# Kernel tuning notes

Hardware: AMD Instinct MI355X
Metric: run time of the kernel (lower is better)

Reference implementation:

```python
import jax, jax.numpy as jnp
import numpy as np

NUM_GROUPS = 16
MINIS_PER_GROUP = 16
MINIS_PER_TOK = 4
HIDDEN = 8192
N_TOKENS = 8192


def setup_inputs() -> dict:
    key = jax.random.key(0)
    k1, k2, k3 = jax.random.split(key, 3)
    hidden_states = jax.random.normal(k1, (N_TOKENS, HIDDEN), dtype=jnp.float32)
    # nn.Linear weight: [num_groups, hidden]
    group_gate_w = jax.random.normal(k2, (NUM_GROUPS, HIDDEN), dtype=jnp.float32) * 0.02
    # mini_gates parameter: [num_groups, hidden, minis_per_group]
    mini_gates = jax.random.normal(k3, (NUM_GROUPS, HIDDEN, MINIS_PER_GROUP), dtype=jnp.float32) * 0.02
    return {"hidden_states": hidden_states, "group_gate_w": group_gate_w, "mini_gates": mini_gates}


def reference(hidden_states, group_gate_w, mini_gates):
    # Tier 1: group gate
    group_logits = hidden_states @ group_gate_w.T                      # [N, G]
    group_probs = jax.nn.softmax(group_logits.astype(jnp.float32), axis=-1)
    top_group_probs = jnp.max(group_probs, axis=-1)                    # [N]
    top_group_indices = jnp.argmax(group_probs, axis=-1)               # [N]

    # Tier 2: per-token mini-gate. Instead of gathering a huge [N, H, E]
    # tensor (as the torch code does), compute logits for ALL groups
    # ([N, G, E] is tiny) and select the chosen group's row — same math.
    all_mini_logits = jnp.einsum('nh,ghe->nge', hidden_states, mini_gates)  # [N, G, E]
    mini_logits = jnp.take_along_axis(
        all_mini_logits, top_group_indices[:, None, None], axis=1
    )[:, 0, :]                                                         # [N, E]
    mini_probs = jax.nn.softmax(mini_logits.astype(jnp.float32), axis=-1)

    topk_mini_probs, topk_mini_indices = jax.lax.top_k(mini_probs, MINIS_PER_TOK)
    final_probs = top_group_probs[:, None] * topk_mini_probs
    final_probs = final_probs / jnp.sum(final_probs, axis=-1, keepdims=True)

    global_expert_indices = top_group_indices[:, None] * MINIS_PER_GROUP + topk_mini_indices

    group_aux_loss = jnp.sum(jnp.mean(group_probs, axis=0) ** 2)
    mini_aux_loss = jnp.sum(jnp.mean(mini_probs, axis=0) ** 2)
    total_aux_loss = group_aux_loss + mini_aux_loss

    return (final_probs.astype(hidden_states.dtype), global_expert_indices, total_aux_loss)
```

## Files before the change

### kernel.cpp

```cpp
#include <hip/hip_runtime.h>
#include <math.h>

#define N_TOK 8192
#define HID   8192
#define NG    16
#define NE    16
#define KC    512
#define NCHUNK (HID / KC)
#define TPB   8

#define OFF_CNT   0u
#define OFF_GSUM  64u
#define OFF_ESUM  128u
#define OFF_NTIL  192u
#define ZERO_BYTES 256u
#define OFF_GLOG  256u
#define OFF_MLOG  (OFF_GLOG + N_TOK*NG*8)
#define OFF_TOPG  (OFF_MLOG + N_TOK*NE*8)
#define OFF_BUCK  (OFF_TOPG + N_TOK*4)
#define OFF_SCHED (OFF_BUCK + NG*N_TOK*4)
#define OFF_MGT   (OFF_SCHED + 2048*4)

__device__ __forceinline__ void glds16(const float* gp, float* lp) {
    __builtin_amdgcn_global_load_lds(
        (const __attribute__((address_space(1))) void*)gp,
        (__attribute__((address_space(3))) void*)lp, 16, 0, 0);
}

#define RS_ROUND(o, half)                                                 \
  {                                                                       \
    const bool hi_ = (lane & (o)) != 0;                                   \
    _Pragma("unroll")                                                     \
    for (int i_ = 0; i_ < (half); ++i_) {                                 \
      double s_ = hi_ ? acc64[i_] : acc64[i_ + (half)];                   \
      double r_ = __shfl_xor(s_, (o));                                    \
      acc64[i_] = (hi_ ? acc64[i_ + (half)] : acc64[i_]) + r_;            \
    }                                                                     \
  }

__global__ __launch_bounds__(256, 2) void k_group(
    const float* __restrict__ hid, const float* __restrict__ gw,
    double* __restrict__ glog)
{
    __shared__ float Wl[2][NG * KC];
    const int tid  = threadIdx.x;
    const int lane = tid & 63;
    const int wv   = tid >> 6;
    const int t0   = blockIdx.x * TPB + wv * 2;
    const float* __restrict__ a0 = hid + (size_t)t0 * HID;
    const float* __restrict__ a1 = a0 + HID;

    #pragma unroll
    for (int j = 0; j < 8; ++j) {
        int m = wv * 8 + j;
        glds16(gw + (size_t)(m >> 1) * HID + (m & 1) * 256 + 4 * lane,
               &Wl[0][m * 256]);
    }
    float4 areg[4];
    areg[0] = *(const float4*)&a0[4 * lane];
    areg[1] = *(const float4*)&a0[256 + 4 * lane];
    areg[2] = *(const float4*)&a1[4 * lane];
    areg[3] = *(const float4*)&a1[256 + 4 * lane];

    double acc64[32];
    #pragma unroll
    for (int i = 0; i < 32; ++i) acc64[i] = 0.0;

    for (int c = 0; c < NCHUNK; ++c) {
        __syncthreads();
        float4 aC0 = areg[0], aC1 = areg[1], aC2 = areg[2], aC3 = areg[3];
        if (c + 1 < NCHUNK) {
            const int kb = (c + 1) * KC;
            #pragma unroll
            for (int j = 0; j < 8; ++j) {
                int m = wv * 8 + j;
                glds16(gw + (size_t)(m >> 1) * HID + kb + (m & 1) * 256 + 4 * lane,
                       &Wl[(c + 1) & 1][m * 256]);
            }
            areg[0] = *(const float4*)&a0[kb + 4 * lane];
            areg[1] = *(const float4*)&a0[kb + 256 + 4 * lane];
            areg[2] = *(const float4*)&a1[kb + 4 * lane];
            areg[3] = *(const float4*)&a1[kb + 256 + 4 * lane];
        }
        const float* Wc = &Wl[c & 1][0];
        #pragma unroll
        for (int g = 0; g < NG; ++g) {
            float4 w0 = *(const float4*)&Wc[g * KC + 4 * lane];
            float4 w1 = *(const float4*)&Wc[g * KC + 256 + 4 * lane];
            float d0 = aC0.x*w0.x + aC0.y*w0.y + aC0.z*w0.z + aC0.w*w0.w
                     + aC1.x*w1.x + aC1.y*w1.y + aC1.z*w1.z + aC1.w*w1.w;
            float d1 = aC2.x*w0.x + aC2.y*w0.y + aC2.z*w0.z + aC2.w*w0.w
                     + aC3.x*w1.x + aC3.y*w1.y + aC3.z*w1.z + aC3.w*w1.w;
            acc64[g]      += (double)d0;
            acc64[16 + g] += (double)d1;
        }
    }

    #pragma unroll
    for (int i = 0; i < 32; ++i) acc64[i] += __shfl_xor(acc64[i], 32);
    RS_ROUND(16, 16) RS_ROUND(8, 8) RS_ROUND(4, 4) RS_ROUND(2, 2) RS_ROUND(1, 1)
    if (lane < 32)
        glog[(size_t)(t0 + (lane >> 4)) * NG + (lane & 15)] = acc64[0];
}

__global__ __launch_bounds__(256) void k_tr(
    const float* __restrict__ mg, float* __restrict__ mgT)
{
    int id = blockIdx.x * 256 + threadIdx.x;
    int g  = id >> 15;
    int r  = id & 32767;
    int e  = r >> 11;
    int kq = r & 2047;
    const float* src = mg + (size_t)g * HID * NE + (size_t)(4 * kq) * NE + e;
    float4 v;
    v.x = src[0]; v.y = src[NE]; v.z = src[2 * NE]; v.w = src[3 * NE];
    *(float4*)&mgT[(size_t)(g * NE + e) * HID + 4 * kq] = v;
}

__global__ __launch_bounds__(64) void k_route(
    const double* __restrict__ glog, int* __restrict__ cnt,
    int* __restrict__ buckets, int* __restrict__ topg, float* __restrict__ gsum)
{
    int t = blockIdx.x * 64 + threadIdx.x;
    float v[NG];
    #pragma unroll
    for (int g = 0; g < NG; ++g) v[g] = (float)glog[t * NG + g];
    float m = v[0];
    #pragma unroll
    for (int g = 1; g < NG; ++g) m = fmaxf(m, v[g]);
    float p[NG], s = 0.f;
    #pragma unroll
    for (int g = 0; g < NG; ++g) { p[g] = expf(v[g] - m); s += p[g]; }
    float inv = 1.f / s;
    #pragma unroll
    for (int g = 0; g < NG; ++g) p[g] *= inv;

    int gi = 0; float best = v[0];
    #pragma unroll
    for (int g = 1; g < NG; ++g) if (v[g] > best) { best = v[g]; gi = g; }

    int lane = threadIdx.x & 63;
    #pragma unroll
    for (int g = 0; g < NG; ++g) {
        float x = p[g];
        #pragma unroll
        for (int off = 32; off > 0; off >>= 1) x += __shfl_down(x, off);
        if (lane == 0) unsafeAtomicAdd(&gsum[g], x);
    }
    topg[t] = gi;
    int pos = atomicAdd(&cnt[gi], 1);
    buckets[gi * N_TOK + pos] = t;
}

__global__ void k_sched(const int* __restrict__ cnt, int* __restrict__ sched,
                        int* __restrict__ ntile)
{
    __shared__ int pref[NG + 1];
    if (threadIdx.x == 0) {
        int s = 0;
        for (int g = 0; g < NG; ++g) { pref[g] = s; s += (cnt[g] + TPB - 1) / TPB; }
        pref[NG] = s; *ntile = s;
    }
    __syncthreads();
    int total = pref[NG];
    for (int i = threadIdx.x; i < total; i += blockDim.x) {
        int g = 0;
        while (g < NG - 1 && i >= pref[g + 1]) ++g;
        sched[i] = (g << 16) | (i - pref[g]);
    }
}

__global__ __launch_bounds__(256, 2) void k_mini(
    const float* __restrict__ hid, const float* __restrict__ mgT,
    const int* __restrict__ cnt, const int* __restrict__ buckets,
    const int* __restrict__ sched, const int* __restrict__ ntile,
    double* __restrict__ mlog)
{
    if ((int)blockIdx.x >= *ntile) return;
    const int enc  = sched[blockIdx.x];
    const int g    = enc >> 16;
    const int tile = enc & 0xffff;
    const int n    = cnt[g] - tile * TPB;

    __shared__ float Wl[2][NE * KC];
    __shared__ int rows[TPB];
    const int tid  = threadIdx.x;
    const int lane = tid & 63;
    const int wv   = tid >> 6;

    if (tid < TPB)
        rows[tid] = buckets[g * N_TOK + tile * TPB + min(tid, n - 1)];
    __syncthreads();
    const float* __restrict__ a0 = hid + (size_t)rows[wv * 2]     * HID;
    const float* __restrict__ a1 = hid + (size_t)rows[wv * 2 + 1] * HID;
    const float* __restrict__ wg = mgT + (size_t)g * NE * HID;

    #pragma unroll
    for (int j = 0; j < 8; ++j) {
        int m = wv * 8 + j;
        glds16(wg + (size_t)(m >> 1) * HID + (m & 1) * 256 + 4 * lane,
               &Wl[0][m * 256]);
    }
    float4 areg[4];
    areg[0] = *(const float4*)&a0[4 * lane];
    areg[1] = *(const float4*)&a0[256 + 4 * lane];
    areg[2] = *(const float4*)&a1[4 * lane];
    areg[3] = *(const float4*)&a1[256 + 4 * lane];

    double acc64[32];
    #pragma unroll
    for (int i = 0; i < 32; ++i) acc64[i] = 0.0;

    for (int c = 0; c < NCHUNK; ++c) {
        __syncthreads();
        float4 aC0 = areg[0], aC1 = areg[1], aC2 = areg[2], aC3 = areg[3];
        if (c + 1 < NCHUNK) {
            const int kb = (c + 1) * KC;
            #pragma unroll
            for (int j = 0; j < 8; ++j) {
                int m = wv * 8 + j;
                glds16(wg + (size_t)(m >> 1) * HID + kb + (m & 1) * 256 + 4 * lane,
                       &Wl[(c + 1) & 1][m * 256]);
            }
            areg[0] = *(const float4*)&a0[kb + 4 * lane];
            areg[1] = *(const float4*)&a0[kb + 256 + 4 * lane];
            areg[2] = *(const float4*)&a1[kb + 4 * lane];
            areg[3] = *(const float4*)&a1[kb + 256 + 4 * lane];
        }
        const float* Wc = &Wl[c & 1][0];
        #pragma unroll
        for (int e = 0; e < NE; ++e) {
            float4 w0 = *(const float4*)&Wc[e * KC + 4 * lane];
            float4 w1 = *(const float4*)&Wc[e * KC + 256 + 4 * lane];
            float d0 = aC0.x*w0.x + aC0.y*w0.y + aC0.z*w0.z + aC0.w*w0.w
                     + aC1.x*w1.x + aC1.y*w1.y + aC1.z*w1.z + aC1.w*w1.w;
            float d1 = aC2.x*w0.x + aC2.y*w0.y + aC2.z*w0.z + aC2.w*w0.w
                     + aC3.x*w1.x + aC3.y*w1.y + aC3.z*w1.z + aC3.w*w1.w;
            acc64[e]      += (double)d0;
            acc64[16 + e] += (double)d1;
        }
    }

    #pragma unroll
    for (int i = 0; i < 32; ++i) acc64[i] += __shfl_xor(acc64[i], 32);
    RS_ROUND(16, 16) RS_ROUND(8, 8) RS_ROUND(4, 4) RS_ROUND(2, 2) RS_ROUND(1, 1)
    if (lane < 32) {
        int tl = wv * 2 + (lane >> 4);
        if (tl < n)
            mlog[(size_t)rows[tl] * NE + (lane & 15)] = acc64[0];
    }
}

__global__ __launch_bounds__(64) void k_final(
    const double* __restrict__ mlog, const int* __restrict__ topg,
    float* __restrict__ out, float* __restrict__ esum)
{
    int t = blockIdx.x * 64 + threadIdx.x;
    float v[NE];
    #pragma unroll
    for (int e = 0; e < NE; ++e) v[e] = (float)mlog[t * NE + e];
    float m = v[0];
    #pragma unroll
    for (int e = 1; e < NE; ++e) m = fmaxf(m, v[e]);
    float p[NE], s = 0.f;
    #pragma unroll
    for (int e = 0; e < NE; ++e) { p[e] = expf(v[e] - m); s += p[e]; }
    float inv = 1.f / s;
    #pragma unroll
    for (int e = 0; e < NE; ++e) p[e] *= inv;

    int lane = threadIdx.x & 63;
    #pragma unroll
    for (int e = 0; e < NE; ++e) {
        float x = p[e];
        #pragma unroll
        for (int off = 32; off > 0; off >>= 1) x += __shfl_down(x, off);
        if (lane == 0) unsafeAtomicAdd(&esum[e], x);
    }

    unsigned used = 0;
    float tv[4]; int ti[4];
    #pragma unroll
    for (int j = 0; j < 4; ++j) {
        float best = -1.f; int bi = 0;
        #pragma unroll
        for (int e = 0; e < NE; ++e)
            if (!((used >> e) & 1u) && p[e] > best) { best = p[e]; bi = e; }
        used |= 1u << bi; tv[j] = best; ti[j] = bi;
    }
    float inv4 = 1.f / (tv[0] + tv[1] + tv[2] + tv[3]);
    int g = topg[t];
    #pragma unroll
    for (int j = 0; j < 4; ++j) {
        out[t * 4 + j]             = tv[j] * inv4;
        out[N_TOK * 4 + t * 4 + j] = (float)(g * NE + ti[j]);
    }
}

__global__ void k_aux(const float* __restrict__ gsum, const float* __restrict__ esum,
                      float* __restrict__ out)
{
    if (threadIdx.x == 0) {
        float a = 0.f;
        for (int g = 0; g < NG; ++g) { float m = gsum[g] * (1.f / N_TOK); a += m * m; }
        for (int e = 0; e < NE; ++e) { float m = esum[e] * (1.f / N_TOK); a += m * m; }
        out[N_TOK * 8] = a;
    }
}

extern "C" void kernel_launch(void* const* d_in, const int* in_sizes, int n_in,
                              void* d_out, int out_size, void* d_ws, size_t ws_size,
                              hipStream_t stream) {
    const float* hid = (const float*)d_in[0];
    const float* gw  = (const float*)d_in[1];
    const float* mg  = (const float*)d_in[2];
    float* out = (float*)d_out;
    char*  ws  = (char*)d_ws;
    int*    cnt     = (int*)   (ws + OFF_CNT);
    float*  gsum    = (float*) (ws + OFF_GSUM);
    float*  esum    = (float*) (ws + OFF_ESUM);
    int*    ntile   = (int*)   (ws + OFF_NTIL);
    double* glog    = (double*)(ws + OFF_GLOG);
    double* mlog    = (double*)(ws + OFF_MLOG);
    int*    topg    = (int*)   (ws + OFF_TOPG);
    int*    buckets = (int*)   (ws + OFF_BUCK);
    int*    sched   = (int*)   (ws + OFF_SCHED);
    float*  mgT     = (float*) (ws + OFF_MGT);

    hipMemsetAsync(d_ws, 0, ZERO_BYTES, stream);

    k_tr<<<2048, 256, 0, stream>>>(mg, mgT);
    k_group<<<N_TOK / TPB, 256, 0, stream>>>(hid, gw, glog);
    k_route<<<N_TOK / 64, 64, 0, stream>>>(glog, cnt, buckets, topg, gsum);
    k_sched<<<1, 256, 0, stream>>>(cnt, sched, ntile);
    k_mini<<<N_TOK / TPB + NG, 256, 0, stream>>>(hid, mgT, cnt, buckets, sched, ntile, mlog);
    k_final<<<N_TOK / 64, 64, 0, stream>>>(mlog, topg, out, esum);
    k_aux<<<1, 64, 0, stream>>>(gsum, esum, out);
}
```

Measured before the change: 574.5 us.

## Fuse routing and final softmax/top-k into GEMV kernels, four tokens per wave

Each wave now processes four tokens instead of two, so every LDS weight tile is reused across more rows and the grid is halved. The group softmax, argmax, bucketing and aux sums move into k_group's epilogue, and the mini softmax, top-k and output writes move into k_mini's, which removes k_route, k_final and the double-precision logit buffers. The transpose kernel's indexing is also reorganised for more coalesced reads. Doubling the double accumulators to 64 per thread raises register pressure and may lower occupancy, and bucket tiles of 16 waste more work on partially filled tiles.

```diff
diff --git a/kernel.cpp b/kernel.cpp
--- a/kernel.cpp
+++ b/kernel.cpp
@@ -7,17 +7,14 @@
 #define NE    16
 #define KC    512
 #define NCHUNK (HID / KC)
-#define TPB   8
+#define TPB   16
 
 #define OFF_CNT   0u
 #define OFF_GSUM  64u
 #define OFF_ESUM  128u
 #define OFF_NTIL  192u
 #define ZERO_BYTES 256u
-#define OFF_GLOG  256u
-#define OFF_MLOG  (OFF_GLOG + N_TOK*NG*8)
-#define OFF_TOPG  (OFF_MLOG + N_TOK*NE*8)
-#define OFF_BUCK  (OFF_TOPG + N_TOK*4)
+#define OFF_BUCK  256u
 #define OFF_SCHED (OFF_BUCK + NG*N_TOK*4)
 #define OFF_MGT   (OFF_SCHED + 2048*4)
 
@@ -38,17 +35,21 @@
     }                                                                     \
   }
 
+#define DOT8(t, w0, w1)                                                   \
+    (aC[2*(t)].x*(w0).x + aC[2*(t)].y*(w0).y + aC[2*(t)].z*(w0).z +       \
+     aC[2*(t)].w*(w0).w + aC[2*(t)+1].x*(w1).x + aC[2*(t)+1].y*(w1).y +   \
+     aC[2*(t)+1].z*(w1).z + aC[2*(t)+1].w*(w1).w)
+
 __global__ __launch_bounds__(256, 2) void k_group(
     const float* __restrict__ hid, const float* __restrict__ gw,
-    double* __restrict__ glog)
+    int* __restrict__ cnt, int* __restrict__ buckets, float* __restrict__ gsum)
 {
     __shared__ float Wl[2][NG * KC];
     const int tid  = threadIdx.x;
     const int lane = tid & 63;
     const int wv   = tid >> 6;
-    const int t0   = blockIdx.x * TPB + wv * 2;
+    const int t0   = blockIdx.x * TPB + wv * 4;
     const float* __restrict__ a0 = hid + (size_t)t0 * HID;
-    const float* __restrict__ a1 = a0 + HID;
 
     #pragma unroll
     for (int j = 0; j < 8; ++j) {
@@ -56,19 +57,22 @@
         glds16(gw + (size_t)(m >> 1) * HID + (m & 1) * 256 + 4 * lane,
                &Wl[0][m * 256]);
     }
-    float4 areg[4];
-    areg[0] = *(const float4*)&a0[4 * lane];
-    areg[1] = *(const float4*)&a0[256 + 4 * lane];
-    areg[2] = *(const float4*)&a1[4 * lane];
-    areg[3] = *(const float4*)&a1[256 + 4 * lane];
-
-    double acc64[32];
-    #pragma unroll
-    for (int i = 0; i < 32; ++i) acc64[i] = 0.0;
+    float4 areg[8];
+    #pragma unroll
+    for (int t = 0; t < 4; ++t) {
+        areg[2*t]   = *(const float4*)&a0[(size_t)t * HID + 4 * lane];
+        areg[2*t+1] = *(const float4*)&a0[(size_t)t * HID + 256 + 4 * lane];
+    }
+
+    double acc64[64];
+    #pragma unroll
+    for (int i = 0; i < 64; ++i) acc64[i] = 0.0;
 
     for (int c = 0; c < NCHUNK; ++c) {
         __syncthreads();
-        float4 aC0 = areg[0], aC1 = areg[1], aC2 = areg[2], aC3 = areg[3];
+        float4 aC[8];
+        #pragma unroll
+        for (int i = 0; i < 8; ++i) aC[i] = areg[i];
         if (c + 1 < NCHUNK) {
             const int kb = (c + 1) * KC;
             #pragma unroll
@@ -77,79 +81,67 @@
                 glds16(gw + (size_t)(m >> 1) * HID + kb + (m & 1) * 256 + 4 * lane,
                        &Wl[(c + 1) & 1][m * 256]);
             }
-            areg[0] = *(const float4*)&a0[kb + 4 * lane];
-            areg[1] = *(const float4*)&a0[kb + 256 + 4 * lane];
-            areg[2] = *(const float4*)&a1[kb + 4 * lane];
-            areg[3] = *(const float4*)&a1[kb + 256 + 4 * lane];
+            #pragma unroll
+            for (int t = 0; t < 4; ++t) {
+                areg[2*t]   = *(const float4*)&a0[(size_t)t * HID + kb + 4 * lane];
+                areg[2*t+1] = *(const float4*)&a0[(size_t)t * HID + kb + 256 + 4 * lane];
+            }
         }
         const float* Wc = &Wl[c & 1][0];
         #pragma unroll
         for (int g = 0; g < NG; ++g) {
             float4 w0 = *(const float4*)&Wc[g * KC + 4 * lane];
             float4 w1 = *(const float4*)&Wc[g * KC + 256 + 4 * lane];
-            float d0 = aC0.x*w0.x + aC0.y*w0.y + aC0.z*w0.z + aC0.w*w0.w
-                     + aC1.x*w1.x + aC1.y*w1.y + aC1.z*w1.z + aC1.w*w1.w;
-            float d1 = aC2.x*w0.x + aC2.y*w0.y + aC2.z*w0.z + aC2.w*w0.w
-                     + aC3.x*w1.x + aC3.y*w1.y + aC3.z*w1.z + aC3.w*w1.w;
-            acc64[g]      += (double)d0;
-            acc64[16 + g] += (double)d1;
-        }
-    }
-
-    #pragma unroll
-    for (int i = 0; i < 32; ++i) acc64[i] += __shfl_xor(acc64[i], 32);
-    RS_ROUND(16, 16) RS_ROUND(8, 8) RS_ROUND(4, 4) RS_ROUND(2, 2) RS_ROUND(1, 1)
-    if (lane < 32)
-        glog[(size_t)(t0 + (lane >> 4)) * NG + (lane & 15)] = acc64[0];
+            #pragma unroll
+            for (int t = 0; t < 4; ++t)
+                acc64[t * 16 + g] += (double)DOT8(t, w0, w1);
+        }
+    }
+
+    RS_ROUND(32, 32) RS_ROUND(16, 16) RS_ROUND(8, 8)
+    RS_ROUND(4, 4)   RS_ROUND(2, 2)   RS_ROUND(1, 1)
+    float v = (float)acc64[0];
+    float mx = v;
+    #pragma unroll
+    for (int o = 8; o; o >>= 1) mx = fmaxf(mx, __shfl_xor(mx, o));
+    float p = expf(v - mx);
+    float s = p;
+    #pragma unroll
+    for (int o = 8; o; o >>= 1) s += __shfl_xor(s, o);
+    p /= s;
+    float x = p;
+    x += __shfl_xor(x, 16);
+    x += __shfl_xor(x, 32);
+    if (lane < 16) unsafeAtomicAdd(&gsum[lane], x);
+    int gi = lane & 15; float bv = v;
+    #pragma unroll
+    for (int o = 8; o; o >>= 1) {
+        float ov = __shfl_xor(bv, o);
+        int   og = __shfl_xor(gi, o);
+        if (ov > bv || (ov == bv && og < gi)) { bv = ov; gi = og; }
+    }
+    if ((lane & 15) == 0) {
+        int t = t0 + (lane >> 4);
+        int pos = atomicAdd(&cnt[gi], 1);
+        buckets[gi * N_TOK + pos] = t;
+    }
 }
 
 __global__ __launch_bounds__(256) void k_tr(
     const float* __restrict__ mg, float* __restrict__ mgT)
 {
-    int id = blockIdx.x * 256 + threadIdx.x;
-    int g  = id >> 15;
-    int r  = id & 32767;
-    int e  = r >> 11;
-    int kq = r & 2047;
-    const float* src = mg + (size_t)g * HID * NE + (size_t)(4 * kq) * NE + e;
+    const int g  = blockIdx.x >> 7;
+    const int kb = (blockIdx.x & 127) * 64;
+    const int e  = threadIdx.x & 15;
+    const int kq = threadIdx.x >> 4;
+    const int k0 = kb + 4 * kq;
+    const float* src = mg + (size_t)g * HID * NE;
     float4 v;
-    v.x = src[0]; v.y = src[NE]; v.z = src[2 * NE]; v.w = src[3 * NE];
-    *(float4*)&mgT[(size_t)(g * NE + e) * HID + 4 * kq] = v;
-}
-
-__global__ __launch_bounds__(64) void k_route(
-    const double* __restrict__ glog, int* __restrict__ cnt,
-    int* __restrict__ buckets, int* __restrict__ topg, float* __restrict__ gsum)
-{
-    int t = blockIdx.x * 64 + threadIdx.x;
-    float v[NG];
-    #pragma unroll
-    for (int g = 0; g < NG; ++g) v[g] = (float)glog[t * NG + g];
-    float m = v[0];
-    #pragma unroll
-    for (int g = 1; g < NG; ++g) m = fmaxf(m, v[g]);
-    float p[NG], s = 0.f;
-    #pragma unroll
-    for (int g = 0; g < NG; ++g) { p[g] = expf(v[g] - m); s += p[g]; }
-    float inv = 1.f / s;
-    #pragma unroll
-    for (int g = 0; g < NG; ++g) p[g] *= inv;
-
-    int gi = 0; float best = v[0];
-    #pragma unroll
-    for (int g = 1; g < NG; ++g) if (v[g] > best) { best = v[g]; gi = g; }
-
-    int lane = threadIdx.x & 63;
-    #pragma unroll
-    for (int g = 0; g < NG; ++g) {
-        float x = p[g];
-        #pragma unroll
-        for (int off = 32; off > 0; off >>= 1) x += __shfl_down(x, off);
-        if (lane == 0) unsafeAtomicAdd(&gsum[g], x);
-    }
-    topg[t] = gi;
-    int pos = atomicAdd(&cnt[gi], 1);
-    buckets[gi * N_TOK + pos] = t;
+    v.x = src[(size_t)(k0 + 0) * NE + e];
+    v.y = src[(size_t)(k0 + 1) * NE + e];
+    v.z = src[(size_t)(k0 + 2) * NE + e];
+    v.w = src[(size_t)(k0 + 3) * NE + e];
+    *(float4*)&mgT[(size_t)(g * NE + e) * HID + k0] = v;
 }
 
 __global__ void k_sched(const int* __restrict__ cnt, int* __restrict__ sched,
@@ -174,7 +166,7 @@
     const float* __restrict__ hid, const float* __restrict__ mgT,
     const int* __restrict__ cnt, const int* __restrict__ buckets,
     const int* __restrict__ sched, const int* __restrict__ ntile,
-    double* __restrict__ mlog)
+    float* __restrict__ out, float* __restrict__ esum)
 {
     if ((int)blockIdx.x >= *ntile) return;
     const int enc  = sched[blockIdx.x];
@@ -183,16 +175,11 @@
     const int n    = cnt[g] - tile * TPB;
 
     __shared__ float Wl[2][NE * KC];
-    __shared__ int rows[TPB];
+    __shared__ int   rows[TPB];
+    __shared__ float sm[256];
     const int tid  = threadIdx.x;
     const int lane = tid & 63;
     const int wv   = tid >> 6;
-
-    if (tid < TPB)
-        rows[tid] = buckets[g * N_TOK + tile * TPB + min(tid, n - 1)];
-    __syncthreads();
-    const float* __restrict__ a0 = hid + (size_t)rows[wv * 2]     * HID;
-    const float* __restrict__ a1 = hid + (size_t)rows[wv * 2 + 1] * HID;
     const float* __restrict__ wg = mgT + (size_t)g * NE * HID;
 
     #pragma unroll
@@ -201,19 +188,28 @@
         glds16(wg + (size_t)(m >> 1) * HID + (m & 1) * 256 + 4 * lane,
                &Wl[0][m * 256]);
     }
-    float4 areg[4];
-    areg[0] = *(const float4*)&a0[4 * lane];
-    areg[1] = *(const float4*)&a0[256 + 4 * lane];
-    areg[2] = *(const float4*)&a1[4 * lane];
-    areg[3] = *(const float4*)&a1[256 + 4 * lane];
-
-    double acc64[32];
-    #pragma unroll
-    for (int i = 0; i < 32; ++i) acc64[i] = 0.0;
+    if (tid < TPB)
+        rows[tid] = buckets[g * N_TOK + tile * TPB + min(tid, n - 1)];
+    __syncthreads();
+    const float* at[4];
+    #pragma unroll
+    for (int t = 0; t < 4; ++t) at[t] = hid + (size_t)rows[wv * 4 + t] * HID;
+
+    float4 areg[8];
+    #pragma unroll
+    for (int t = 0; t < 4; ++t) {
+        areg[2*t]   = *(const float4*)&at[t][4 * lane];
+        areg[2*t+1] = *(const float4*)&at[t][256 + 4 * lane];
+    }
+    double acc64[64];
+    #pragma unroll
+    for (int i = 0; i < 64; ++i) acc64[i] = 0.0;
 
     for (int c = 0; c < NCHUNK; ++c) {
         __syncthreads();
-        float4 aC0 = areg[0], aC1 = areg[1], aC2 = areg[2], aC3 = areg[3];
+        float4 aC[8];
+        #pragma unroll
+        for (int i = 0; i < 8; ++i) aC[i] = areg[i];
         if (c + 1 < NCHUNK) {
             const int kb = (c + 1) * KC;
             #pragma unroll
@@ -222,78 +218,66 @@
                 glds16(wg + (size_t)(m >> 1) * HID + kb + (m & 1) * 256 + 4 * lane,
                        &Wl[(c + 1) & 1][m * 256]);
             }
-            areg[0] = *(const float4*)&a0[kb + 4 * lane];
-            areg[1] = *(const float4*)&a0[kb + 256 + 4 * lane];
-            areg[2] = *(const float4*)&a1[kb + 4 * lane];
-            areg[3] = *(const float4*)&a1[kb + 256 + 4 * lane];
+            #pragma unroll
+            for (int t = 0; t < 4; ++t) {
+                areg[2*t]   = *(const float4*)&at[t][kb + 4 * lane];
+                areg[2*t+1] = *(const float4*)&at[t][kb + 256 + 4 * lane];
+            }
         }
         const float* Wc = &Wl[c & 1][0];
         #pragma unroll
         for (int e = 0; e < NE; ++e) {
             float4 w0 = *(const float4*)&Wc[e * KC + 4 * lane];
             float4 w1 = *(const float4*)&Wc[e * KC + 256 + 4 * lane];
-            float d0 = aC0.x*w0.x + aC0.y*w0.y + aC0.z*w0.z + aC0.w*w0.w
-                     + aC1.x*w1.x + aC1.y*w1.y + aC1.z*w1.z + aC1.w*w1.w;
-            float d1 = aC2.x*w0.x + aC2.y*w0.y + aC2.z*w0.z + aC2.w*w0.w
-                     + aC3.x*w1.x + aC3.y*w1.y + aC3.z*w1.z + aC3.w*w1.w;
-            acc64[e]      += (double)d0;
-            acc64[16 + e] += (double)d1;
-        }
-    }
-
-    #pragma unroll
-    for (int i = 0; i < 32; ++i) acc64[i] += __shfl_xor(acc64[i], 32);
-    RS_ROUND(16, 16) RS_ROUND(8, 8) RS_ROUND(4, 4) RS_ROUND(2, 2) RS_ROUND(1, 1)
-    if (lane < 32) {
-        int tl = wv * 2 + (lane >> 4);
-        if (tl < n)
-            mlog[(size_t)rows[tl] * NE + (lane & 15)] = acc64[0];
-    }
-}
-
-__global__ __launch_bounds__(64) void k_final(
-    const double* __restrict__ mlog, const int* __restrict__ topg,
-    float* __restrict__ out, float* __restrict__ esum)
-{
-    int t = blockIdx.x * 64 + threadIdx.x;
-    float v[NE];
-    #pragma unroll
-    for (int e = 0; e < NE; ++e) v[e] = (float)mlog[t * NE + e];
-    float m = v[0];
-    #pragma unroll
-    for (int e = 1; e < NE; ++e) m = fmaxf(m, v[e]);
-    float p[NE], s = 0.f;
-    #pragma unroll
-    for (int e = 0; e < NE; ++e) { p[e] = expf(v[e] - m); s += p[e]; }
-    float inv = 1.f / s;
-    #pragma unroll
-    for (int e = 0; e < NE; ++e) p[e] *= inv;
-
-    int lane = threadIdx.x & 63;
-    #pragma unroll
-    for (int e = 0; e < NE; ++e) {
-        float x = p[e];
-        #pragma unroll
-        for (int off = 32; off > 0; off >>= 1) x += __shfl_down(x, off);
-        if (lane == 0) unsafeAtomicAdd(&esum[e], x);
-    }
-
-    unsigned used = 0;
-    float tv[4]; int ti[4];
-    #pragma unroll
-    for (int j = 0; j < 4; ++j) {
-        float best = -1.f; int bi = 0;
-        #pragma unroll
-        for (int e = 0; e < NE; ++e)
-            if (!((used >> e) & 1u) && p[e] > best) { best = p[e]; bi = e; }
-        used |= 1u << bi; tv[j] = best; ti[j] = bi;
-    }
-    float inv4 = 1.f / (tv[0] + tv[1] + tv[2] + tv[3]);
-    int g = topg[t];
-    #pragma unroll
-    for (int j = 0; j < 4; ++j) {
-        out[t * 4 + j]             = tv[j] * inv4;
-        out[N_TOK * 4 + t * 4 + j] = (float)(g * NE + ti[j]);
+            #pragma unroll
+            for (int t = 0; t < 4; ++t)
+                acc64[t * 16 + e] += (double)DOT8(t, w0, w1);
+        }
+    }
+
+    RS_ROUND(32, 32) RS_ROUND(16, 16) RS_ROUND(8, 8)
+    RS_ROUND(4, 4)   RS_ROUND(2, 2)   RS_ROUND(1, 1)
+    const int tl = wv * 4 + (lane >> 4);
+    float v = (float)acc64[0];
+    float mx = v;
+    #pragma unroll
+    for (int o = 8; o; o >>= 1) mx = fmaxf(mx, __shfl_xor(mx, o));
+    float p = expf(v - mx);
+    float s = p;
+    #pragma unroll
+    for (int o = 8; o; o >>= 1) s += __shfl_xor(s, o);
+    p /= s;
+    float x = (tl < n) ? p : 0.f;
+    x += __shfl_xor(x, 16);
+    x += __shfl_xor(x, 32);
+    if (lane < 16) unsafeAtomicAdd(&esum[lane], x);
+
+    sm[tid] = p;
+    __syncthreads();
+    if ((tid & 15) == 0) {
+        int tt = tid >> 4;
+        if (tt < n) {
+            float pe[NE];
+            #pragma unroll
+            for (int e = 0; e < NE; ++e) pe[e] = sm[tt * 16 + e];
+            unsigned used = 0;
+            float tv[4]; int ti[4];
+            #pragma unroll
+            for (int j = 0; j < 4; ++j) {
+                float best = -1.f; int bi = 0;
+                #pragma unroll
+                for (int e = 0; e < NE; ++e)
+                    if (!((used >> e) & 1u) && pe[e] > best) { best = pe[e]; bi = e; }
+                used |= 1u << bi; tv[j] = best; ti[j] = bi;
+            }
+            float inv4 = 1.f / (tv[0] + tv[1] + tv[2] + tv[3]);
+            int t = rows[tt];
+            #pragma unroll
+            for (int j = 0; j < 4; ++j) {
+                out[t * 4 + j]             = tv[j] * inv4;
+                out[N_TOK * 4 + t * 4 + j] = (float)(g * NE + ti[j]);
+            }
+        }
     }
 }
 
@@ -320,9 +304,6 @@
     float*  gsum    = (float*) (ws + OFF_GSUM);
     float*  esum    = (float*) (ws + OFF_ESUM);
     int*    ntile   = (int*)   (ws + OFF_NTIL);
-    double* glog    = (double*)(ws + OFF_GLOG);
-    double* mlog    = (double*)(ws + OFF_MLOG);
-    int*    topg    = (int*)   (ws + OFF_TOPG);
     int*    buckets = (int*)   (ws + OFF_BUCK);
     int*    sched   = (int*)   (ws + OFF_SCHED);
     float*  mgT     = (float*) (ws + OFF_MGT);
@@ -330,10 +311,8 @@
     hipMemsetAsync(d_ws, 0, ZERO_BYTES, stream);
 
     k_tr<<<2048, 256, 0, stream>>>(mg, mgT);
-    k_group<<<N_TOK / TPB, 256, 0, stream>>>(hid, gw, glog);
-    k_route<<<N_TOK / 64, 64, 0, stream>>>(glog, cnt, buckets, topg, gsum);
+    k_group<<<N_TOK / TPB, 256, 0, stream>>>(hid, gw, cnt, buckets, gsum);
     k_sched<<<1, 256, 0, stream>>>(cnt, sched, ntile);
-    k_mini<<<N_TOK / TPB + NG, 256, 0, stream>>>(hid, mgT, cnt, buckets, sched, ntile, mlog);
-    k_final<<<N_TOK / 64, 64, 0, stream>>>(mlog, topg, out, esum);
+    k_mini<<<N_TOK / TPB + NG, 256, 0, stream>>>(hid, mgT, cnt, buckets, sched, ntile, out, esum);
     k_aux<<<1, 64, 0, stream>>>(gsum, esum, out);
 }
```

Measured after the change: 537.5 us. 1.07x faster.
